# Optimization experiments

Hardware: AMD Instinct MI355X
Metric: run time of the kernel (lower is better)

Reference implementation:

```python
import jax, jax.numpy as jnp
import numpy as np

N_NODES = 100000
N_EDGES = 1200000
N_FEAT = 128
HIDDEN = 64
N_CLASSES = 40


def setup_inputs() -> dict:
    key = jax.random.key(0)
    k1, k2, k3, k4 = jax.random.split(key, 4)
    x = jax.random.normal(k1, (N_NODES, N_FEAT), dtype=jnp.float32)
    edge_index = jax.random.randint(k2, (2, N_EDGES), 0, N_NODES, dtype=jnp.int64)
    # Glorot-style init for the linear weights (as in PyG GCNConv)
    W1 = jax.random.normal(k3, (N_FEAT, HIDDEN), dtype=jnp.float32) * (1.0 / np.sqrt(N_FEAT))
    b1 = jnp.zeros((HIDDEN,), dtype=jnp.float32)
    W2 = jax.random.normal(k4, (HIDDEN, N_CLASSES), dtype=jnp.float32) * (1.0 / np.sqrt(HIDDEN))
    b2 = jnp.zeros((N_CLASSES,), dtype=jnp.float32)
    return {"x": x, "edge_index": edge_index, "W1": W1, "b1": b1, "W2": W2, "b2": b2}


def _gcn_conv(x, row, col, dinv, W, b):
    # x: [N, Fin], W: [Fin, Fout]. Transform then normalized scatter-add aggregation.
    h = x @ W                                  # [N, Fout]
    norm = dinv[row] * dinv[col]               # [E'] symmetric normalization
    msgs = h[row] * norm[:, None]              # [E', Fout] gather + scale
    out = jax.ops.segment_sum(msgs, col, num_segments=x.shape[0])  # scatter-add
    return out + b


def reference(x, edge_index, W1, b1, W2, b2):
    N = x.shape[0]
    loops = jnp.arange(N, dtype=edge_index.dtype)
    # add self loops (PyG GCNConv default)
    row = jnp.concatenate([edge_index[0], loops])
    col = jnp.concatenate([edge_index[1], loops])
    deg = jax.ops.segment_sum(jnp.ones_like(col, dtype=x.dtype), col, num_segments=N)
    dinv = jax.lax.rsqrt(deg)  # deg >= 1 thanks to self loops
    h = jax.nn.relu(_gcn_conv(x, row, col, dinv, W1, b1))
    # dropout is identity at inference (training=False)
    return _gcn_conv(h, row, col, dinv, W2, b2)
```

## Files before the change

### kernel.cpp

```cpp
#include <hip/hip_runtime.h>
#include <hip/hip_fp16.h>
#include <type_traits>

#define N_NODES 100000
#define N_EDGES 1200000
#define N_FEAT 128
#define HIDDEN 64
#define N_CLASSES 40

#define BSHIFT 9
#define BMASK 511
#define BUCKET_NODES 512
#define NBK ((N_NODES + BUCKET_NODES - 1) / BUCKET_NODES)
#define BCAP 8192
#define CHUNK 2048

typedef _Float16 f16x8 __attribute__((ext_vector_type(8)));
typedef float f32x4 __attribute__((ext_vector_type(4)));


__global__ __launch_bounds__(256) void bucket_kernel(const int* __restrict__ row,
                                                     const int* __restrict__ col,
                                                     int* __restrict__ gcursor,
                                                     unsigned* __restrict__ bke, int E) {
    __shared__ int hist[NBK];
    __shared__ int pfx[NBK];
    __shared__ int gbase[NBK];
    __shared__ int lcnt[NBK];
    __shared__ unsigned ord[CHUNK];
    __shared__ unsigned char obkt[CHUNK];

    const int t = threadIdx.x;
    const int e0 = blockIdx.x * CHUNK;
    const int nE = min(CHUNK, E - e0);

    for (int i = t; i < NBK; i += 256) {
        hist[i] = 0;
        lcnt[i] = 0;
    }
    __syncthreads();

    for (int i = t; i < nE; i += 256) atomicAdd(&hist[col[e0 + i] >> BSHIFT], 1);
    __syncthreads();

    int v = (t < NBK) ? hist[t] : 0;
    if (t < NBK) pfx[t] = v;
    __syncthreads();
    for (int d = 1; d < 256; d <<= 1) {
        int add = (t >= d && t < NBK) ? pfx[t - d] : 0;
        __syncthreads();
        if (t < NBK) pfx[t] += add;
        __syncthreads();
    }
    if (t < NBK) {
        pfx[t] -= v;
        gbase[t] = t * BCAP + ((v > 0) ? atomicAdd(&gcursor[t], v) : 0);
    }
    __syncthreads();

    for (int i = t; i < nE; i += 256) {
        int r = row[e0 + i];
        int c = col[e0 + i];
        int b = c >> BSHIFT;
        int pos = pfx[b] + atomicAdd(&lcnt[b], 1);
        ord[pos] = ((unsigned)r << BSHIFT) | (unsigned)(c & BMASK);
        obkt[pos] = (unsigned char)b;
    }
    __syncthreads();

    for (int i = t; i < nE; i += 256) {
        int b = obkt[i];
        bke[(size_t)gbase[b] + (i - pfx[b])] = ord[i];
    }
}


__global__ __launch_bounds__(256) void place_kernel(const int* __restrict__ gcursor,
                                                    const unsigned* __restrict__ bke,
                                                    int* __restrict__ rowptr,
                                                    float* __restrict__ dinv,
                                                    int* __restrict__ csr_src, int n) {
    __shared__ int hist[BUCKET_NODES];
    __shared__ int cur[BUCKET_NODES];
    __shared__ int tsum[256];

    const int b = blockIdx.x, t = threadIdx.x;
    const int node0 = b << BSHIFT;
    const int nNodes = min(BUCKET_NODES, n - node0);

    const int myCnt = (t < NBK) ? gcursor[t] : 0;
    tsum[t] = myCnt;
    __syncthreads();
    for (int d = 1; d < 256; d <<= 1) {
        int add = (t >= d) ? tsum[t - d] : 0;
        __syncthreads();
        tsum[t] += add;
        __syncthreads();
    }
    const int base = tsum[b] - gcursor[b];
    const int nb = gcursor[b];
    __syncthreads();

    hist[t] = 0;
    hist[t + 256] = 0;
    __syncthreads();

    const unsigned* src = bke + (size_t)b * BCAP;
    for (int i = t; i < nb; i += 256) atomicAdd(&hist[src[i] & BMASK], 1);
    __syncthreads();

    const int c0 = hist[2 * t];
    const int c1 = hist[2 * t + 1];
    const int s = c0 + c1;
    tsum[t] = s;
    __syncthreads();
    for (int d = 1; d < 256; d <<= 1) {
        int add = (t >= d) ? tsum[t - d] : 0;
        __syncthreads();
        tsum[t] += add;
        __syncthreads();
    }
    const int e0 = base + tsum[t] - s;
    const int e1 = e0 + c0;

    cur[2 * t] = e0;
    cur[2 * t + 1] = e1;
    if (2 * t < nNodes) {
        rowptr[node0 + 2 * t] = e0;
        dinv[node0 + 2 * t] = rsqrtf((float)(c0 + 1));
    }
    if (2 * t + 1 < nNodes) {
        rowptr[node0 + 2 * t + 1] = e1;
        dinv[node0 + 2 * t + 1] = rsqrtf((float)(c1 + 1));
    }
    if (t == 0 && node0 + nNodes == n) rowptr[n] = N_EDGES;
    __syncthreads();

    for (int i = t; i < nb; i += 256) {
        unsigned p = src[i];
        int pos = atomicAdd(&cur[p & BMASK], 1);
        csr_src[pos] = (int)(p >> BSHIFT);
    }
}


template <typename XT, int K, int XSTRIDE, int NOUT, int NOUT_PAD, int OSTRIDE>
__global__ __launch_bounds__(256) void gemm_mfma_kernel(const XT* __restrict__ X,
                                                        const float* __restrict__ W,
                                                        const float* __restrict__ dinv,
                                                        __half* __restrict__ Hs, int M) {
    constexpr int KCH = K / 32;
    constexpr int NT = NOUT_PAD / 16;
    constexpr int WPITCH = NOUT_PAD + 2;

    __shared__ _Float16 wh[K * WPITCH];
    __shared__ float sdinv[256];

    const int tid = threadIdx.x;
    const int bnode0 = blockIdx.x * 256;

    for (int i = tid; i < K * NOUT_PAD; i += 256) {
        int k = i / NOUT_PAD, n = i % NOUT_PAD;
        wh[k * WPITCH + n] = (n < NOUT) ? (_Float16)W[k * NOUT + n] : (_Float16)0.0f;
    }
    {
        int node = bnode0 + tid;
        sdinv[tid] = (node < M) ? dinv[node] : 0.f;
    }
    __syncthreads();

    const int wid = tid >> 6;
    const int lane = tid & 63;
    const int m = lane & 15;
    const int quad = lane >> 4;

    f16x8 bf[KCH][NT];
#pragma unroll
    for (int kc = 0; kc < KCH; ++kc)
#pragma unroll
        for (int nt = 0; nt < NT; ++nt)
#pragma unroll
            for (int j = 0; j < 8; ++j)
                bf[kc][nt][j] = wh[(kc * 32 + quad * 8 + j) * WPITCH + nt * 16 + m];

    for (int nt4 = 0; nt4 < 4; ++nt4) {
        const int nb = bnode0 + wid * 64 + nt4 * 16;
        if (nb >= M) break;
        const int rowi = min(nb + m, M - 1);
        const XT* xr = X + (size_t)rowi * XSTRIDE;

        f32x4 acc[NT];
#pragma unroll
        for (int nt = 0; nt < NT; ++nt) acc[nt] = (f32x4){0.f, 0.f, 0.f, 0.f};

#pragma unroll
        for (int kc = 0; kc < KCH; ++kc) {
            f16x8 af;
            if constexpr (std::is_same<XT, float>::value) {
                float4 u0 = *(const float4*)&xr[kc * 32 + quad * 8];
                float4 u1 = *(const float4*)&xr[kc * 32 + quad * 8 + 4];
                af[0] = (_Float16)u0.x;
                af[1] = (_Float16)u0.y;
                af[2] = (_Float16)u0.z;
                af[3] = (_Float16)u0.w;
                af[4] = (_Float16)u1.x;
                af[5] = (_Float16)u1.y;
                af[6] = (_Float16)u1.z;
                af[7] = (_Float16)u1.w;
            } else {
                af = *(const f16x8*)&xr[kc * 32 + quad * 8];
            }
#pragma unroll
            for (int nt = 0; nt < NT; ++nt)
                acc[nt] = __builtin_amdgcn_mfma_f32_16x16x32_f16(af, bf[kc][nt], acc[nt], 0, 0, 0);
        }

#pragma unroll
        for (int reg = 0; reg < 4; ++reg) {
            const int node = nb + quad * 4 + reg;
            if (node < M) {
                const float s = sdinv[node - bnode0];
#pragma unroll
                for (int nt = 0; nt < NT; ++nt) {
                    const int f = nt * 16 + m;
                    if (NOUT == NOUT_PAD || f < NOUT)
                        Hs[(size_t)node * OSTRIDE + f] = __float2half(acc[nt][reg] * s);
                }
            }
        }
    }
}


__device__ inline void acc_mix16(float (&acc)[8], uint4 u, float one) {
    const unsigned* w = (const unsigned*)&u;
#pragma unroll
    for (int k = 0; k < 4; ++k) {
        asm("v_fma_mix_f32 %0, %1, %2, %0 op_sel:[0,0,0] op_sel_hi:[1,0,0]"
            : "+v"(acc[2 * k])
            : "v"(w[k]), "v"(one));
        asm("v_fma_mix_f32 %0, %1, %2, %0 op_sel:[1,0,0] op_sel_hi:[1,0,0]"
            : "+v"(acc[2 * k + 1])
            : "v"(w[k]), "v"(one));
    }
}

template <typename OutT, int FCHUNKS, int HSTRIDE, int OUTSTRIDE, bool RELU>
__global__ __launch_bounds__(256) void gather_g8_kernel(const int* __restrict__ rowptr,
                                                        const int* __restrict__ csr_src,
                                                        const float* __restrict__ dinv,
                                                        const __half* __restrict__ hs,
                                                        const float* __restrict__ bias,
                                                        OutT* __restrict__ out, int n) {
    const int wave = (blockIdx.x * blockDim.x + threadIdx.x) >> 6;
    const int lane = threadIdx.x & 63;
    const int g = lane >> 3;
    const int q = lane & 7;
    const int c = wave * 8 + g;
    if (c >= n || q >= FCHUNKS) return;

    const float one = 1.0f;
    const int eBeg = rowptr[c];
    const int eEnd = rowptr[c + 1];

    float acc[8];
#pragma unroll
    for (int j = 0; j < 8; ++j) acc[j] = 0.f;

    const __half* hq = hs + q * 8;

    acc_mix16(acc, *(const uint4*)(hq + (size_t)c * HSTRIDE), one);

    int e = eBeg;
    for (; e + 2 <= eEnd; e += 2) {
        int r0 = csr_src[e];
        int r1 = csr_src[e + 1];
        uint4 u0 = *(const uint4*)(hq + (size_t)r0 * HSTRIDE);
        uint4 u1 = *(const uint4*)(hq + (size_t)r1 * HSTRIDE);
        acc_mix16(acc, u0, one);
        acc_mix16(acc, u1, one);
    }
    if (e < eEnd) {
        int r = csr_src[e];
        acc_mix16(acc, *(const uint4*)(hq + (size_t)r * HSTRIDE), one);
    }

    const float dc = dinv[c];
    float o[8];
#pragma unroll
    for (int j = 0; j < 8; ++j) {
        float v = fmaf(acc[j], dc, bias[q * 8 + j]);
        o[j] = RELU ? fmaxf(v, 0.f) : v;
    }

    if constexpr (std::is_same<OutT, float>::value) {
        float* dst = &out[(size_t)c * OUTSTRIDE + q * 8];
        *(float4*)dst = make_float4(o[0], o[1], o[2], o[3]);
        *(float4*)(dst + 4) = make_float4(o[4], o[5], o[6], o[7]);
    } else {
        __half2 pk[4];
#pragma unroll
        for (int k = 0; k < 4; ++k) pk[k] = __floats2half2_rn(o[2 * k], o[2 * k + 1]);
        *(uint4*)&out[(size_t)c * OUTSTRIDE + q * 8] = *(uint4*)pk;
    }
}


extern "C" void kernel_launch(void* const* d_in, const int* in_sizes, int n_in,
                              void* d_out, int out_size, void* d_ws, size_t ws_size,
                              hipStream_t stream) {
    const float* x = (const float*)d_in[0];
    const int* row = (const int*)d_in[1];
    const int* col = row + N_EDGES;
    const float* W1 = (const float*)d_in[2];
    const float* b1 = (const float*)d_in[3];
    const float* W2 = (const float*)d_in[4];
    const float* b2 = (const float*)d_in[5];
    float* out = (float*)d_out;

    const int N = N_NODES, E = N_EDGES;

    char* p = (char*)d_ws;
    auto alloc = [&](size_t bytes) {
        char* q = p;
        p += (bytes + 255) & ~(size_t)255;
        return q;
    };
    int* rowptr = (int*)alloc((size_t)(N + 1) * 4);
    int* csr_src = (int*)alloc((size_t)E * 4);
    int* gcursor = (int*)alloc((size_t)NBK * 4);
    unsigned* bke = (unsigned*)alloc((size_t)NBK * BCAP * 4);
    float* dinv = (float*)alloc((size_t)N * 4);
    __half* h1s = (__half*)alloc((size_t)N * HIDDEN * 2);
    __half* agg1h = (__half*)alloc((size_t)N * HIDDEN * 2);
    __half* h2s = (__half*)alloc((size_t)N * N_CLASSES * 2);

    hipMemsetAsync(gcursor, 0, (size_t)NBK * 4, stream);
    bucket_kernel<<<(E + CHUNK - 1) / CHUNK, 256, 0, stream>>>(row, col, gcursor, bke, E);
    place_kernel<<<NBK, 256, 0, stream>>>(gcursor, bke, rowptr, dinv, csr_src, N);

    gemm_mfma_kernel<float, N_FEAT, N_FEAT, HIDDEN, HIDDEN, HIDDEN>
        <<<(N + 255) / 256, 256, 0, stream>>>(x, W1, dinv, h1s, N);
    gather_g8_kernel<__half, 8, HIDDEN, HIDDEN, true>
        <<<(N + 31) / 32, 256, 0, stream>>>(rowptr, csr_src, dinv, h1s, b1, agg1h, N);

    gemm_mfma_kernel<_Float16, HIDDEN, HIDDEN, N_CLASSES, 48, N_CLASSES>
        <<<(N + 255) / 256, 256, 0, stream>>>((const _Float16*)agg1h, W2, dinv, h2s, N);
    gather_g8_kernel<float, 5, N_CLASSES, N_CLASSES, false>
        <<<(N + 31) / 32, 256, 0, stream>>>(rowptr, csr_src, dinv, h2s, b2, out, N);
}
```

Measured before the change: 215.9 us.

## Sort nodes by degree within buckets and pack 12 nodes per wave in layer-2 gather

The place kernel now counting-sorts each 512-node bucket by in-degree (capped at 63) and writes a node permutation, so each wave of the gather kernels processes nodes of similar degree and suffers less loop divergence. The layer-2 gather also packs 12 nodes of 5 lanes into a wave instead of 8 nodes of 8 lanes, leaving fewer lanes idle. In exchange the place kernel does an extra scan, the gathers add an indirection through gorder, and output writes become scattered.

```diff
diff --git a/kernel.cpp b/kernel.cpp
--- a/kernel.cpp
+++ b/kernel.cpp
@@ -79,10 +79,13 @@
                                                     const unsigned* __restrict__ bke,
                                                     int* __restrict__ rowptr,
                                                     float* __restrict__ dinv,
-                                                    int* __restrict__ csr_src, int n) {
+                                                    int* __restrict__ csr_src,
+                                                    int* __restrict__ gorder, int n) {
     __shared__ int hist[BUCKET_NODES];
     __shared__ int cur[BUCKET_NODES];
     __shared__ int tsum[256];
+    __shared__ int dh[64];
+    __shared__ int dbase[64];
 
     const int b = blockIdx.x, t = threadIdx.x;
     const int node0 = b << BSHIFT;
@@ -103,6 +106,7 @@
 
     hist[t] = 0;
     hist[t + 256] = 0;
+    if (t < 64) dh[t] = 0;
     __syncthreads();
 
     const unsigned* src = bke + (size_t)b * BCAP;
@@ -134,6 +138,27 @@
         dinv[node0 + 2 * t + 1] = rsqrtf((float)(c1 + 1));
     }
     if (t == 0 && node0 + nNodes == n) rowptr[n] = N_EDGES;
+
+    const int d0 = min(c0, 63);
+    const int d1 = min(c1, 63);
+    int p0 = 0, p1 = 0;
+    if (2 * t < nNodes) p0 = atomicAdd(&dh[d0], 1);
+    if (2 * t + 1 < nNodes) p1 = atomicAdd(&dh[d1], 1);
+    __syncthreads();
+
+    if (t < 64) tsum[t] = dh[t];
+    __syncthreads();
+    for (int d = 1; d < 64; d <<= 1) {
+        int add = (t >= d && t < 64) ? tsum[t - d] : 0;
+        __syncthreads();
+        if (t < 64) tsum[t] += add;
+        __syncthreads();
+    }
+    if (t < 64) dbase[t] = tsum[t] - dh[t];
+    __syncthreads();
+
+    if (2 * t < nNodes) gorder[node0 + dbase[d0] + p0] = node0 + 2 * t;
+    if (2 * t + 1 < nNodes) gorder[node0 + dbase[d1] + p1] = node0 + 2 * t + 1;
     __syncthreads();
 
     for (int i = t; i < nb; i += 256) {
@@ -245,8 +270,9 @@
     }
 }
 
-template <typename OutT, int FCHUNKS, int HSTRIDE, int OUTSTRIDE, bool RELU>
-__global__ __launch_bounds__(256) void gather_g8_kernel(const int* __restrict__ rowptr,
+template <typename OutT, int NG, int FCHUNKS, int HSTRIDE, int OUTSTRIDE, bool RELU>
+__global__ __launch_bounds__(256) void gather_g8_kernel(const int* __restrict__ gorder,
+                                                        const int* __restrict__ rowptr,
                                                         const int* __restrict__ csr_src,
                                                         const float* __restrict__ dinv,
                                                         const __half* __restrict__ hs,
@@ -254,10 +280,12 @@
                                                         OutT* __restrict__ out, int n) {
     const int wave = (blockIdx.x * blockDim.x + threadIdx.x) >> 6;
     const int lane = threadIdx.x & 63;
-    const int g = lane >> 3;
-    const int q = lane & 7;
-    const int c = wave * 8 + g;
-    if (c >= n || q >= FCHUNKS) return;
+    if (NG * FCHUNKS < 64 && lane >= NG * FCHUNKS) return;
+    const int g = lane / FCHUNKS;
+    const int q = lane % FCHUNKS;
+    const int idx = wave * NG + g;
+    if (idx >= n) return;
+    const int c = gorder[idx];
 
     const float one = 1.0f;
     const int eBeg = rowptr[c];
@@ -331,21 +359,22 @@
     int* gcursor = (int*)alloc((size_t)NBK * 4);
     unsigned* bke = (unsigned*)alloc((size_t)NBK * BCAP * 4);
     float* dinv = (float*)alloc((size_t)N * 4);
+    int* gorder = (int*)alloc((size_t)N * 4);
     __half* h1s = (__half*)alloc((size_t)N * HIDDEN * 2);
     __half* agg1h = (__half*)alloc((size_t)N * HIDDEN * 2);
     __half* h2s = (__half*)alloc((size_t)N * N_CLASSES * 2);
 
     hipMemsetAsync(gcursor, 0, (size_t)NBK * 4, stream);
     bucket_kernel<<<(E + CHUNK - 1) / CHUNK, 256, 0, stream>>>(row, col, gcursor, bke, E);
-    place_kernel<<<NBK, 256, 0, stream>>>(gcursor, bke, rowptr, dinv, csr_src, N);
+    place_kernel<<<NBK, 256, 0, stream>>>(gcursor, bke, rowptr, dinv, csr_src, gorder, N);
 
     gemm_mfma_kernel<float, N_FEAT, N_FEAT, HIDDEN, HIDDEN, HIDDEN>
         <<<(N + 255) / 256, 256, 0, stream>>>(x, W1, dinv, h1s, N);
-    gather_g8_kernel<__half, 8, HIDDEN, HIDDEN, true>
-        <<<(N + 31) / 32, 256, 0, stream>>>(rowptr, csr_src, dinv, h1s, b1, agg1h, N);
+    gather_g8_kernel<__half, 8, 8, HIDDEN, HIDDEN, true>
+        <<<(N + 31) / 32, 256, 0, stream>>>(gorder, rowptr, csr_src, dinv, h1s, b1, agg1h, N);
 
     gemm_mfma_kernel<_Float16, HIDDEN, HIDDEN, N_CLASSES, 48, N_CLASSES>
         <<<(N + 255) / 256, 256, 0, stream>>>((const _Float16*)agg1h, W2, dinv, h2s, N);
-    gather_g8_kernel<float, 5, N_CLASSES, N_CLASSES, false>
-        <<<(N + 31) / 32, 256, 0, stream>>>(rowptr, csr_src, dinv, h2s, b2, out, N);
-}
+    gather_g8_kernel<float, 12, 5, N_CLASSES, N_CLASSES, false>
+        <<<(N + 47) / 48, 256, 0, stream>>>(gorder, rowptr, csr_src, dinv, h2s, b2, out, N);
+}
```

After: 232.9 us. 7.9% more time.

## Process two destination nodes per lane group in gather kernels and repack lanes

Applied to the files above, without the earlier changes.

The gather kernel now has each lane group accumulate two destination nodes at once, interleaving their neighbor loads so more independent memory requests are in flight per lane. For the second layer (40 features, 5 chunks), lanes are repacked into 12 groups of 5 instead of 8 groups of 8, so fewer lanes sit idle. The cost is higher register pressure from two accumulators, imbalance when the two nodes have different degrees, and half as many waves in the grid.

```diff
diff --git a/kernel.cpp b/kernel.cpp
--- a/kernel.cpp
+++ b/kernel.cpp
@@ -245,63 +245,123 @@
     }
 }
 
-template <typename OutT, int FCHUNKS, int HSTRIDE, int OUTSTRIDE, bool RELU>
-__global__ __launch_bounds__(256) void gather_g8_kernel(const int* __restrict__ rowptr,
-                                                        const int* __restrict__ csr_src,
-                                                        const float* __restrict__ dinv,
-                                                        const __half* __restrict__ hs,
-                                                        const float* __restrict__ bias,
-                                                        OutT* __restrict__ out, int n) {
+template <typename OutT, int NGRP, int FCHUNKS, int HSTRIDE, int OUTSTRIDE, bool RELU>
+__global__ __launch_bounds__(256) void gather_pair_kernel(const int* __restrict__ rowptr,
+                                                          const int* __restrict__ csr_src,
+                                                          const float* __restrict__ dinv,
+                                                          const __half* __restrict__ hs,
+                                                          const float* __restrict__ bias,
+                                                          OutT* __restrict__ out, int n) {
     const int wave = (blockIdx.x * blockDim.x + threadIdx.x) >> 6;
     const int lane = threadIdx.x & 63;
-    const int g = lane >> 3;
-    const int q = lane & 7;
-    const int c = wave * 8 + g;
-    if (c >= n || q >= FCHUNKS) return;
+    if (NGRP * FCHUNKS < 64 && lane >= NGRP * FCHUNKS) return;
+    const int g = lane / FCHUNKS;
+    const int q = lane % FCHUNKS;
+    const int base = wave * (2 * NGRP);
+    const int cA = base + g;
+    const int cB = base + NGRP + g;
+    if (cA >= n) return;
+    const bool hasB = (cB < n);
 
     const float one = 1.0f;
-    const int eBeg = rowptr[c];
-    const int eEnd = rowptr[c + 1];
-
-    float acc[8];
-#pragma unroll
-    for (int j = 0; j < 8; ++j) acc[j] = 0.f;
-
     const __half* hq = hs + q * 8;
 
-    acc_mix16(acc, *(const uint4*)(hq + (size_t)c * HSTRIDE), one);
-
-    int e = eBeg;
-    for (; e + 2 <= eEnd; e += 2) {
-        int r0 = csr_src[e];
-        int r1 = csr_src[e + 1];
+    float accA[8], accB[8];
+#pragma unroll
+    for (int j = 0; j < 8; ++j) {
+        accA[j] = 0.f;
+        accB[j] = 0.f;
+    }
+
+    int eA = rowptr[cA];
+    const int endA = rowptr[cA + 1];
+    int eB = 0, endB = 0;
+    if (hasB) {
+        eB = rowptr[cB];
+        endB = rowptr[cB + 1];
+    }
+
+    acc_mix16(accA, *(const uint4*)(hq + (size_t)cA * HSTRIDE), one);
+    if (hasB) acc_mix16(accB, *(const uint4*)(hq + (size_t)cB * HSTRIDE), one);
+
+    while (eA + 2 <= endA && eB + 2 <= endB) {
+        int rA0 = csr_src[eA];
+        int rA1 = csr_src[eA + 1];
+        int rB0 = csr_src[eB];
+        int rB1 = csr_src[eB + 1];
+        uint4 uA0 = *(const uint4*)(hq + (size_t)rA0 * HSTRIDE);
+        uint4 uA1 = *(const uint4*)(hq + (size_t)rA1 * HSTRIDE);
+        uint4 uB0 = *(const uint4*)(hq + (size_t)rB0 * HSTRIDE);
+        uint4 uB1 = *(const uint4*)(hq + (size_t)rB1 * HSTRIDE);
+        acc_mix16(accA, uA0, one);
+        acc_mix16(accA, uA1, one);
+        acc_mix16(accB, uB0, one);
+        acc_mix16(accB, uB1, one);
+        eA += 2;
+        eB += 2;
+    }
+    for (; eA + 2 <= endA; eA += 2) {
+        int r0 = csr_src[eA];
+        int r1 = csr_src[eA + 1];
         uint4 u0 = *(const uint4*)(hq + (size_t)r0 * HSTRIDE);
         uint4 u1 = *(const uint4*)(hq + (size_t)r1 * HSTRIDE);
-        acc_mix16(acc, u0, one);
-        acc_mix16(acc, u1, one);
-    }
-    if (e < eEnd) {
-        int r = csr_src[e];
-        acc_mix16(acc, *(const uint4*)(hq + (size_t)r * HSTRIDE), one);
-    }
-
-    const float dc = dinv[c];
-    float o[8];
-#pragma unroll
-    for (int j = 0; j < 8; ++j) {
-        float v = fmaf(acc[j], dc, bias[q * 8 + j]);
-        o[j] = RELU ? fmaxf(v, 0.f) : v;
-    }
-
-    if constexpr (std::is_same<OutT, float>::value) {
-        float* dst = &out[(size_t)c * OUTSTRIDE + q * 8];
-        *(float4*)dst = make_float4(o[0], o[1], o[2], o[3]);
-        *(float4*)(dst + 4) = make_float4(o[4], o[5], o[6], o[7]);
-    } else {
-        __half2 pk[4];
-#pragma unroll
-        for (int k = 0; k < 4; ++k) pk[k] = __floats2half2_rn(o[2 * k], o[2 * k + 1]);
-        *(uint4*)&out[(size_t)c * OUTSTRIDE + q * 8] = *(uint4*)pk;
+        acc_mix16(accA, u0, one);
+        acc_mix16(accA, u1, one);
+    }
+    if (eA < endA) {
+        int r = csr_src[eA];
+        acc_mix16(accA, *(const uint4*)(hq + (size_t)r * HSTRIDE), one);
+    }
+    for (; eB + 2 <= endB; eB += 2) {
+        int r0 = csr_src[eB];
+        int r1 = csr_src[eB + 1];
+        uint4 u0 = *(const uint4*)(hq + (size_t)r0 * HSTRIDE);
+        uint4 u1 = *(const uint4*)(hq + (size_t)r1 * HSTRIDE);
+        acc_mix16(accB, u0, one);
+        acc_mix16(accB, u1, one);
+    }
+    if (eB < endB) {
+        int r = csr_src[eB];
+        acc_mix16(accB, *(const uint4*)(hq + (size_t)r * HSTRIDE), one);
+    }
+
+    {
+        const float dc = dinv[cA];
+        float o[8];
+#pragma unroll
+        for (int j = 0; j < 8; ++j) {
+            float v = fmaf(accA[j], dc, bias[q * 8 + j]);
+            o[j] = RELU ? fmaxf(v, 0.f) : v;
+        }
+        if constexpr (std::is_same<OutT, float>::value) {
+            float* dst = &out[(size_t)cA * OUTSTRIDE + q * 8];
+            *(float4*)dst = make_float4(o[0], o[1], o[2], o[3]);
+            *(float4*)(dst + 4) = make_float4(o[4], o[5], o[6], o[7]);
+        } else {
+            __half2 pk[4];
+#pragma unroll
+            for (int k = 0; k < 4; ++k) pk[k] = __floats2half2_rn(o[2 * k], o[2 * k + 1]);
+            *(uint4*)&out[(size_t)cA * OUTSTRIDE + q * 8] = *(uint4*)pk;
+        }
+    }
+    if (hasB) {
+        const float dc = dinv[cB];
+        float o[8];
+#pragma unroll
+        for (int j = 0; j < 8; ++j) {
+            float v = fmaf(accB[j], dc, bias[q * 8 + j]);
+            o[j] = RELU ? fmaxf(v, 0.f) : v;
+        }
+        if constexpr (std::is_same<OutT, float>::value) {
+            float* dst = &out[(size_t)cB * OUTSTRIDE + q * 8];
+            *(float4*)dst = make_float4(o[0], o[1], o[2], o[3]);
+            *(float4*)(dst + 4) = make_float4(o[4], o[5], o[6], o[7]);
+        } else {
+            __half2 pk[4];
+#pragma unroll
+            for (int k = 0; k < 4; ++k) pk[k] = __floats2half2_rn(o[2 * k], o[2 * k + 1]);
+            *(uint4*)&out[(size_t)cB * OUTSTRIDE + q * 8] = *(uint4*)pk;
+        }
     }
 }
 
@@ -341,11 +401,11 @@
 
     gemm_mfma_kernel<float, N_FEAT, N_FEAT, HIDDEN, HIDDEN, HIDDEN>
         <<<(N + 255) / 256, 256, 0, stream>>>(x, W1, dinv, h1s, N);
-    gather_g8_kernel<__half, 8, HIDDEN, HIDDEN, true>
-        <<<(N + 31) / 32, 256, 0, stream>>>(rowptr, csr_src, dinv, h1s, b1, agg1h, N);
+    gather_pair_kernel<__half, 8, 8, HIDDEN, HIDDEN, true>
+        <<<(N + 63) / 64, 256, 0, stream>>>(rowptr, csr_src, dinv, h1s, b1, agg1h, N);
 
     gemm_mfma_kernel<_Float16, HIDDEN, HIDDEN, N_CLASSES, 48, N_CLASSES>
         <<<(N + 255) / 256, 256, 0, stream>>>((const _Float16*)agg1h, W2, dinv, h2s, N);
-    gather_g8_kernel<float, 5, N_CLASSES, N_CLASSES, false>
-        <<<(N + 31) / 32, 256, 0, stream>>>(rowptr, csr_src, dinv, h2s, b2, out, N);
-}
+    gather_pair_kernel<float, 12, 5, N_CLASSES, N_CLASSES, false>
+        <<<(N + 95) / 96, 256, 0, stream>>>(rowptr, csr_src, dinv, h2s, b2, out, N);
+}
```

Result: slower. 222.1 us (+2.9%).

## Fuse layer-1 gather with layer-2 GEMM and pack second gather lanes

Applied to the files above, without the earlier changes.

Merges the first aggregation (with bias and ReLU) and the second dense transform into one kernel. Each 64-node block aggregates its rows into shared memory, then runs an MFMA against W2, which is converted to fp16 in shared memory per block. This removes the agg1h round trip through global memory and one launch. The second gather now packs 12 nodes per wave using 5 lanes each, instead of 8 nodes with 3 idle lanes per group, and h2s uses a padded stride of 48. Rebuilding W2 in LDS in every block adds redundant work, and one block covers 64 nodes, so per-node edge imbalance may limit occupancy.

```diff
diff --git a/kernel.cpp b/kernel.cpp
--- a/kernel.cpp
+++ b/kernel.cpp
@@ -245,19 +245,134 @@
     }
 }
 
-template <typename OutT, int FCHUNKS, int HSTRIDE, int OUTSTRIDE, bool RELU>
-__global__ __launch_bounds__(256) void gather_g8_kernel(const int* __restrict__ rowptr,
-                                                        const int* __restrict__ csr_src,
-                                                        const float* __restrict__ dinv,
-                                                        const __half* __restrict__ hs,
-                                                        const float* __restrict__ bias,
-                                                        OutT* __restrict__ out, int n) {
+
+__global__ __launch_bounds__(256) void gather1_gemm2_kernel(
+    const int* __restrict__ rowptr, const int* __restrict__ csr_src,
+    const float* __restrict__ dinv, const __half* __restrict__ h1s,
+    const float* __restrict__ b1, const float* __restrict__ W2,
+    __half* __restrict__ h2s, int n) {
+    constexpr int APITCH = 72;
+    constexpr int WPITCH = 50;
+
+    __shared__ _Float16 agg[64 * APITCH];
+    __shared__ _Float16 wh[64 * WPITCH];
+    __shared__ float sdinv[64];
+
+    const int tid = threadIdx.x;
+    const int base = blockIdx.x * 64;
+
+    for (int i = tid; i < 64 * 48; i += 256) {
+        int k = i / 48, nn = i % 48;
+        wh[k * WPITCH + nn] = (nn < 40) ? (_Float16)W2[k * 40 + nn] : (_Float16)0.0f;
+    }
+    if (tid < 64) {
+        int node = base + tid;
+        sdinv[tid] = (node < n) ? dinv[node] : 0.f;
+    }
+    __syncthreads();
+
+    const int wid = tid >> 6;
+    const int lane = tid & 63;
+    const int g = lane >> 3;
+    const int q = lane & 7;
+    const float one = 1.0f;
+    const __half* hq = h1s + q * 8;
+
+#pragma unroll
+    for (int t = 0; t < 2; ++t) {
+        const int nl = t * 32 + wid * 8 + g;
+        const int c = base + nl;
+        if (c < n) {
+            float acc[8];
+#pragma unroll
+            for (int j = 0; j < 8; ++j) acc[j] = 0.f;
+
+            acc_mix16(acc, *(const uint4*)(hq + (size_t)c * HIDDEN), one);
+
+            int e = rowptr[c];
+            const int eEnd = rowptr[c + 1];
+            for (; e + 2 <= eEnd; e += 2) {
+                int r0 = csr_src[e];
+                int r1 = csr_src[e + 1];
+                uint4 u0 = *(const uint4*)(hq + (size_t)r0 * HIDDEN);
+                uint4 u1 = *(const uint4*)(hq + (size_t)r1 * HIDDEN);
+                acc_mix16(acc, u0, one);
+                acc_mix16(acc, u1, one);
+            }
+            if (e < eEnd) {
+                int r = csr_src[e];
+                acc_mix16(acc, *(const uint4*)(hq + (size_t)r * HIDDEN), one);
+            }
+
+            const float dc = sdinv[nl];
+            _Float16 hv[8];
+#pragma unroll
+            for (int j = 0; j < 8; ++j) {
+                float v = fmaf(acc[j], dc, b1[q * 8 + j]);
+                hv[j] = (_Float16)fmaxf(v, 0.f);
+            }
+            *(f16x8*)&agg[nl * APITCH + q * 8] = *(f16x8*)hv;
+        }
+    }
+    __syncthreads();
+
+    const int m = lane & 15;
+    const int quad = lane >> 4;
+
+    f16x8 bf[2][3];
+#pragma unroll
+    for (int kc = 0; kc < 2; ++kc)
+#pragma unroll
+        for (int nt = 0; nt < 3; ++nt)
+#pragma unroll
+            for (int j = 0; j < 8; ++j)
+                bf[kc][nt][j] = wh[(kc * 32 + quad * 8 + j) * WPITCH + nt * 16 + m];
+
+    const int nl0 = wid * 16;
+
+    f32x4 acc2[3];
+#pragma unroll
+    for (int nt = 0; nt < 3; ++nt) acc2[nt] = (f32x4){0.f, 0.f, 0.f, 0.f};
+
+#pragma unroll
+    for (int kc = 0; kc < 2; ++kc) {
+        f16x8 af = *(const f16x8*)&agg[(nl0 + m) * APITCH + kc * 32 + quad * 8];
+#pragma unroll
+        for (int nt = 0; nt < 3; ++nt)
+            acc2[nt] = __builtin_amdgcn_mfma_f32_16x16x32_f16(af, bf[kc][nt], acc2[nt], 0, 0, 0);
+    }
+
+#pragma unroll
+    for (int reg = 0; reg < 4; ++reg) {
+        const int nl = nl0 + quad * 4 + reg;
+        const int node = base + nl;
+        if (node < n) {
+            const float s = sdinv[nl];
+#pragma unroll
+            for (int nt = 0; nt < 3; ++nt) {
+                const int f = nt * 16 + m;
+                if (f < N_CLASSES)
+                    h2s[(size_t)node * 48 + f] = __float2half(acc2[nt][reg] * s);
+            }
+        }
+    }
+}
+
+
+template <typename OutT, int NG, int FCHUNKS, int HSTRIDE, int OUTSTRIDE, bool RELU>
+__global__ __launch_bounds__(256) void gather_kernel(const int* __restrict__ rowptr,
+                                                     const int* __restrict__ csr_src,
+                                                     const float* __restrict__ dinv,
+                                                     const __half* __restrict__ hs,
+                                                     const float* __restrict__ bias,
+                                                     OutT* __restrict__ out, int n) {
     const int wave = (blockIdx.x * blockDim.x + threadIdx.x) >> 6;
     const int lane = threadIdx.x & 63;
-    const int g = lane >> 3;
-    const int q = lane & 7;
-    const int c = wave * 8 + g;
-    if (c >= n || q >= FCHUNKS) return;
+    if (NG * FCHUNKS < 64 && lane >= NG * FCHUNKS) return;
+    const int g = lane / FCHUNKS;
+    const int q = lane % FCHUNKS;
+    const int c = wave * NG + g;
+    if (c >= n) return;
 
     const float one = 1.0f;
     const int eBeg = rowptr[c];
@@ -332,8 +447,7 @@
     unsigned* bke = (unsigned*)alloc((size_t)NBK * BCAP * 4);
     float* dinv = (float*)alloc((size_t)N * 4);
     __half* h1s = (__half*)alloc((size_t)N * HIDDEN * 2);
-    __half* agg1h = (__half*)alloc((size_t)N * HIDDEN * 2);
-    __half* h2s = (__half*)alloc((size_t)N * N_CLASSES * 2);
+    __half* h2s = (__half*)alloc((size_t)N * 48 * 2);
 
     hipMemsetAsync(gcursor, 0, (size_t)NBK * 4, stream);
     bucket_kernel<<<(E + CHUNK - 1) / CHUNK, 256, 0, stream>>>(row, col, gcursor, bke, E);
@@ -341,11 +455,10 @@
 
     gemm_mfma_kernel<float, N_FEAT, N_FEAT, HIDDEN, HIDDEN, HIDDEN>
         <<<(N + 255) / 256, 256, 0, stream>>>(x, W1, dinv, h1s, N);
-    gather_g8_kernel<__half, 8, HIDDEN, HIDDEN, true>
-        <<<(N + 31) / 32, 256, 0, stream>>>(rowptr, csr_src, dinv, h1s, b1, agg1h, N);
-
-    gemm_mfma_kernel<_Float16, HIDDEN, HIDDEN, N_CLASSES, 48, N_CLASSES>
-        <<<(N + 255) / 256, 256, 0, stream>>>((const _Float16*)agg1h, W2, dinv, h2s, N);
-    gather_g8_kernel<float, 5, N_CLASSES, N_CLASSES, false>
-        <<<(N + 31) / 32, 256, 0, stream>>>(rowptr, csr_src, dinv, h2s, b2, out, N);
-}
+
+    gather1_gemm2_kernel<<<(N + 63) / 64, 256, 0, stream>>>(rowptr, csr_src, dinv, h1s,
+                                                            b1, W2, h2s, N);
+
+    gather_kernel<float, 12, 5, 48, N_CLASSES, false>
+        <<<(N + 47) / 48, 256, 0, stream>>>(rowptr, csr_src, dinv, h2s, b2, out, N);
+}
```

Result: no change. 212.1 us (-1.8%).
